# Kernel tuning notes

Hardware: AMD Instinct MI355X
Metric: run time of the kernel (lower is better)

The kernel has to match this reference:

```python
import jax, jax.numpy as jnp
import numpy as np

NUM_HEADS = 16


def _rope(x, c, s):
    # x: [T, H, D]; c, s: [T, D/2] -> rotate-half RoPE over full head_dim
    d2 = c.shape[-1]
    x1, x2 = x[..., :d2], x[..., d2:]
    c = c[:, None, :]
    s = s[:, None, :]
    return jnp.concatenate([x1 * c - x2 * s, x2 * c + x1 * s], axis=-1)


def setup_inputs() -> dict:
    key = jax.random.key(0)
    ks = jax.random.split(key, 4)
    B, L, dim = 8, 1024, 1024
    T = B * L
    D = dim // NUM_HEADS
    hidden_states = jax.random.normal(ks[0], (T, dim), dtype=jnp.float32)
    w_qkv = jax.random.normal(ks[1], (dim, 3 * dim), dtype=jnp.float32) * (dim ** -0.5)
    b_qkv = jnp.zeros((3 * dim,), dtype=jnp.float32)
    w_proj = jax.random.normal(ks[2], (dim, dim), dtype=jnp.float32) * (dim ** -0.5)
    b_proj = jnp.zeros((dim,), dtype=jnp.float32)
    # RoPE tables: positions restart at 0 for each packed sequence
    pos = jnp.tile(jnp.arange(L, dtype=jnp.float32), B)  # [T]
    inv_freq = 1.0 / (10000.0 ** (jnp.arange(0, D, 2, dtype=jnp.float32) / D))  # [D/2]
    freqs = pos[:, None] * inv_freq[None, :]  # [T, D/2]
    emb = jnp.concatenate([freqs, freqs], axis=-1)  # [T, D]
    cos = jnp.cos(emb)
    sin = jnp.sin(emb)
    cu_seqlens = (jnp.arange(B + 1, dtype=jnp.int32) * L)
    return {"hidden_states": hidden_states, "cos": cos, "sin": sin,
            "w_qkv": w_qkv, "b_qkv": b_qkv, "w_proj": w_proj, "b_proj": b_proj,
            "cu_seqlens": cu_seqlens}


def reference(hidden_states, cos, sin, w_qkv, b_qkv, w_proj, b_proj, cu_seqlens):
    T, dim = hidden_states.shape
    H = NUM_HEADS
    D = dim // H
    B = cu_seqlens.shape[0] - 1  # equal-length packed sequences
    L = T // B

    qkv = hidden_states @ w_qkv + b_qkv            # [T, 3*dim]
    qkv = qkv.reshape(T, 3, H, D)
    q, k, v = qkv[:, 0], qkv[:, 1], qkv[:, 2]       # [T, H, D]

    # module chunks cos/sin in half along last dim before apply_rotary_emb
    c = cos[..., : D // 2].astype(jnp.float32)
    s = sin[..., : D // 2].astype(jnp.float32)
    q = _rope(q.astype(jnp.float32), c, s).astype(hidden_states.dtype)
    k = _rope(k.astype(jnp.float32), c, s).astype(hidden_states.dtype)

    # varlen flash attention == block-diagonal attention; equal lengths -> reshape
    qb = q.reshape(B, L, H, D)
    kb = k.reshape(B, L, H, D)
    vb = v.reshape(B, L, H, D)
    scale = D ** -0.5
    scores = jnp.einsum("bqhd,bkhd->bhqk", qb, kb) * scale  # [B, H, L, L]
    probs = jax.nn.softmax(scores, axis=-1)
    out = jnp.einsum("bhqk,bkhd->bqhd", probs, vb)           # [B, L, H, D]
    out = out.reshape(T, dim)
    return out @ w_proj + b_proj
```

## Files before the change

### kernel.cpp

```cpp
#include <hip/hip_runtime.h>

typedef unsigned short ushort_t;
typedef __attribute__((ext_vector_type(8))) short short8;
typedef __attribute__((ext_vector_type(4))) float f32x4;

#define AS1 __attribute__((address_space(1)))
#define AS3 __attribute__((address_space(3)))

__device__ __forceinline__ ushort_t f2bf(float f) {
  unsigned int u = __builtin_bit_cast(unsigned int, f);
  u += 0x7fffu + ((u >> 16) & 1u);
  return (ushort_t)(u >> 16);
}

__device__ __forceinline__ unsigned int pack_bf2(float a, float b) {
  unsigned int ua = __builtin_bit_cast(unsigned int, a) + 0x8000u;
  unsigned int ub = __builtin_bit_cast(unsigned int, b) + 0x8000u;
  return (ua >> 16) | (ub & 0xffff0000u);
}

__device__ __forceinline__ void load_lds16(const ushort_t* g, ushort_t* l) {
  __builtin_amdgcn_global_load_lds((AS1 void*)g, (AS3 void*)l, 16, 0, 0);
}

#define MFMA16(a, b, c) __builtin_amdgcn_mfma_f32_16x16x32_bf16((a), (b), (c), 0, 0, 0)

__global__ __launch_bounds__(256) void k_convert(const float* __restrict__ src,
                                                 ushort_t* __restrict__ dst, int n8) {
  int i = blockIdx.x * 256 + threadIdx.x;
  if (i >= n8) return;
  const float4* s4 = (const float4*)src;
  float4 a = s4[(size_t)i * 2], b = s4[(size_t)i * 2 + 1];
  short8 o;
  o[0] = (short)f2bf(a.x); o[1] = (short)f2bf(a.y);
  o[2] = (short)f2bf(a.z); o[3] = (short)f2bf(a.w);
  o[4] = (short)f2bf(b.x); o[5] = (short)f2bf(b.y);
  o[6] = (short)f2bf(b.z); o[7] = (short)f2bf(b.w);
  *(short8*)(dst + (size_t)i * 8) = o;
}

__global__ __launch_bounds__(256) void k_transpose_w(const float* __restrict__ wqkv,
                                                     ushort_t* __restrict__ wqkvT,
                                                     const float* __restrict__ wproj,
                                                     ushort_t* __restrict__ wprojT) {
  __shared__ ushort_t t[64 * 65];
  const float* src;
  ushort_t* dst;
  int C, bx;
  if (blockIdx.x < 48) { src = wqkv; dst = wqkvT; C = 3072; bx = blockIdx.x; }
  else { src = wproj; dst = wprojT; C = 1024; bx = blockIdx.x - 48; }
  const int R = 1024;
  const int x0 = bx * 64, y0 = blockIdx.y * 64;
  const int c = threadIdx.x & 63, r0 = threadIdx.x >> 6;
#pragma unroll
  for (int i = 0; i < 16; ++i) {
    int r = r0 + i * 4;
    t[c * 65 + r] = f2bf(src[(size_t)(y0 + r) * C + x0 + c]);
  }
  __syncthreads();
#pragma unroll
  for (int i = 0; i < 16; ++i) {
    int rr = r0 + i * 4;
    dst[(size_t)(x0 + rr) * R + y0 + c] = t[rr * 65 + c];
  }
}

__global__ __launch_bounds__(512) void k_qkv_gemm_rope(
    const ushort_t* __restrict__ A, const ushort_t* __restrict__ Bt,
    const float* __restrict__ bias, const float* __restrict__ cosb,
    const float* __restrict__ sinb, ushort_t* __restrict__ Qb,
    ushort_t* __restrict__ Kb, ushort_t* __restrict__ Vp) {
  constexpr int K = 1024;
  __shared__ __align__(16) ushort_t As[256 * 64];
  __shared__ __align__(16) ushort_t Bs[128 * 64];
  const int tid = threadIdx.x, lane = tid & 63, wave = tid >> 6;
  const int quad = lane >> 4, ml = lane & 15;
  const int wm = wave & 3, wn = wave >> 2;
  const int m0 = blockIdx.y * 256, n0 = blockIdx.x * 128;
  f32x4 acc[4][4] = {};

  for (int kt = 0; kt < K / 64; ++kt) {
    __syncthreads();
    {
      const int kk0 = kt * 64;
#pragma unroll
      for (int i = 0; i < 4; ++i) {
        int cch = i * 512 + tid;
        int r = cch >> 3, s = cch & 7, gs = s ^ (r & 7);
        load_lds16(A + (size_t)(m0 + r) * K + kk0 + gs * 8, As + cch * 8);
      }
#pragma unroll
      for (int i = 0; i < 2; ++i) {
        int cch = i * 512 + tid;
        int r = cch >> 3, s = cch & 7, gs = s ^ (r & 7);
        load_lds16(Bt + (size_t)(n0 + r) * K + kk0 + gs * 8, Bs + cch * 8);
      }
    }
    __syncthreads();
#pragma unroll
    for (int ks = 0; ks < 2; ++ks) {
      short8 af[4], bfr[4];
#pragma unroll
      for (int mb = 0; mb < 4; ++mb) {
        int row = wm * 64 + mb * 16 + ml;
        int gs = (ks * 4 + quad) ^ (row & 7);
        af[mb] = *(const short8*)(As + row * 64 + gs * 8);
      }
#pragma unroll
      for (int nb = 0; nb < 4; ++nb) {
        int row = wn * 64 + nb * 16 + ml;
        int gs = (ks * 4 + quad) ^ (row & 7);
        bfr[nb] = *(const short8*)(Bs + row * 64 + gs * 8);
      }
#pragma unroll
      for (int mb = 0; mb < 4; ++mb)
#pragma unroll
        for (int nb = 0; nb < 4; ++nb)
          acc[mb][nb] = MFMA16(af[mb], bfr[nb], acc[mb][nb]);
    }
  }

  const int ncol0 = n0 + wn * 64;
  const int sec = ncol0 >> 10;
  const int h = (ncol0 & 1023) >> 6;
  if (sec < 2) {
    ushort_t* dst = (sec == 0) ? Qb : Kb;
#pragma unroll
    for (int mb = 0; mb < 4; ++mb) {
#pragma unroll
      for (int rg = 0; rg < 4; ++rg) {
        const int m = m0 + wm * 64 + mb * 16 + quad * 4 + rg;
        const int b = m >> 10, l = m & 1023;
        const size_t ob = ((size_t)(b * 16 + h) * 1024 + l) * 64;
#pragma unroll
        for (int nb = 0; nb < 2; ++nb) {
          const int d = nb * 16 + ml;
          float x1 = acc[mb][nb][rg] + bias[ncol0 + d];
          float x2 = acc[mb][nb + 2][rg] + bias[ncol0 + d + 32];
          float cv = cosb[(size_t)m * 64 + d];
          float sv = sinb[(size_t)m * 64 + d];
          dst[ob + d] = f2bf(x1 * cv - x2 * sv);
          dst[ob + d + 32] = f2bf(x2 * cv + x1 * sv);
        }
      }
    }
  } else {
    const int mrow = m0 + wm * 64;
    const int b = mrow >> 10, lB = mrow & 1023;
    ushort_t* vb = Vp + ((size_t)(b * 16 + h)) * 65536 + lB;
#pragma unroll
    for (int rg = 0; rg < 4; ++rg) {
#pragma unroll
      for (int nb = 0; nb < 4; ++nb) {
        const int d = nb * 16 + ml;
        const float bs = bias[ncol0 + d];
        uint2 w;
        w.x = pack_bf2(acc[0][nb][rg] + bs, acc[1][nb][rg] + bs);
        w.y = pack_bf2(acc[2][nb][rg] + bs, acc[3][nb][rg] + bs);
        *(uint2*)(vb + (size_t)d * 1024 + 16 * quad + 4 * rg) = w;
      }
    }
  }
}

__global__ __launch_bounds__(256, 4) void k_attn(const ushort_t* __restrict__ Qb,
                                                 const ushort_t* __restrict__ Kb,
                                                 const ushort_t* __restrict__ Vp,
                                                 ushort_t* __restrict__ Ob) {
  __shared__ __align__(16) ushort_t QP[9216];
  __shared__ __align__(16) ushort_t Ks[64 * 64];
  __shared__ __align__(16) ushort_t Vts[64 * 64];
  const int tid = threadIdx.x, lane = tid & 63, wave = tid >> 6;
  const int quad = lane >> 4, ml = lane & 15;
  const int bh = blockIdx.x & 127, qt = blockIdx.x >> 7;
  const int q0 = qt * 128;
  const size_t base = (size_t)bh * 65536;
  const float CEXP = 0.18033688011112042f;

#pragma unroll
  for (int i = 0; i < 4; ++i) {
    int cch = i * 256 + tid;
    int r = cch >> 3, s = cch & 7, gs = s ^ (r & 7);
    load_lds16(Qb + base + (size_t)(q0 + r) * 64 + gs * 8, QP + cch * 8);
  }
  __syncthreads();

  short8 qf[2][2];
#pragma unroll
  for (int mb = 0; mb < 2; ++mb)
#pragma unroll
    for (int ks = 0; ks < 2; ++ks) {
      int row = wave * 32 + mb * 16 + ml;
      int gs = (ks * 4 + quad) ^ (row & 7);
      qf[mb][ks] = *(const short8*)(QP + row * 64 + gs * 8);
    }

  ushort_t* Pw = QP + wave * 2304;
  f32x4 Oacc[2][4] = {};
  float lsum[2][4] = {};

  for (int kt = 0; kt < 16; ++kt) {
    __syncthreads();
#pragma unroll
    for (int i = 0; i < 2; ++i) {
      int cch = i * 256 + tid;
      int r = cch >> 3, s = cch & 7, gs = s ^ (r & 7);
      load_lds16(Kb + base + (size_t)(kt * 64 + r) * 64 + gs * 8, Ks + cch * 8);
    }
#pragma unroll
    for (int i = 0; i < 2; ++i) {
      int cch = i * 256 + tid;
      int r = cch >> 3, s = cch & 7, gs = s ^ (r & 7);
      load_lds16(Vp + base + (size_t)r * 1024 + kt * 64 + gs * 8, Vts + cch * 8);
    }
    __syncthreads();

    f32x4 Sacc[2][4] = {};
#pragma unroll
    for (int nb = 0; nb < 4; ++nb)
#pragma unroll
      for (int ks = 0; ks < 2; ++ks) {
        int row = nb * 16 + ml;
        int gs = (ks * 4 + quad) ^ (row & 7);
        short8 kf = *(const short8*)(Ks + row * 64 + gs * 8);
        Sacc[0][nb] = MFMA16(qf[0][ks], kf, Sacc[0][nb]);
        Sacc[1][nb] = MFMA16(qf[1][ks], kf, Sacc[1][nb]);
      }

#pragma unroll
    for (int mb = 0; mb < 2; ++mb) {
#pragma unroll
      for (int rg = 0; rg < 4; ++rg) {
        float p0 = exp2f(Sacc[mb][0][rg] * CEXP);
        float p1 = exp2f(Sacc[mb][1][rg] * CEXP);
        float p2 = exp2f(Sacc[mb][2][rg] * CEXP);
        float p3 = exp2f(Sacc[mb][3][rg] * CEXP);
        lsum[mb][rg] += (p0 + p1) + (p2 + p3);
        uint2 w;
        w.x = pack_bf2(p0, p1);
        w.y = pack_bf2(p2, p3);
        *(uint2*)(Pw + (mb * 16 + quad * 4 + rg) * 72 + ml * 4) = w;
      }
    }

#pragma unroll
    for (int ks = 0; ks < 2; ++ks) {
      short8 pf[2];
#pragma unroll
      for (int mb = 0; mb < 2; ++mb)
        pf[mb] = *(const short8*)(Pw + (mb * 16 + ml) * 72 + ks * 32 + quad * 8);
#pragma unroll
      for (int nb = 0; nb < 4; ++nb) {
        int row = nb * 16 + ml;
        int gs = (ks * 4 + quad) ^ (row & 7);
        short8 vf = *(const short8*)(Vts + row * 64 + gs * 8);
        Oacc[0][nb] = MFMA16(pf[0], vf, Oacc[0][nb]);
        Oacc[1][nb] = MFMA16(pf[1], vf, Oacc[1][nb]);
      }
    }
  }

  const int b = bh >> 4, h = bh & 15;
#pragma unroll
  for (int mb = 0; mb < 2; ++mb) {
#pragma unroll
    for (int rg = 0; rg < 4; ++rg) {
      float l = lsum[mb][rg];
      l += __shfl_xor(l, 1);
      l += __shfl_xor(l, 2);
      l += __shfl_xor(l, 4);
      l += __shfl_xor(l, 8);
      float inv = 1.f / l;
      int q = q0 + wave * 32 + mb * 16 + quad * 4 + rg;
      size_t ob = ((size_t)(b * 1024 + q)) * 1024 + h * 64;
#pragma unroll
      for (int nb = 0; nb < 4; ++nb)
        Ob[ob + nb * 16 + ml] = f2bf(Oacc[mb][nb][rg] * inv);
    }
  }
}

__global__ __launch_bounds__(256) void k_proj_gemm(const ushort_t* __restrict__ A,
                                                   const ushort_t* __restrict__ Bt,
                                                   const float* __restrict__ bias,
                                                   float* __restrict__ out) {
  constexpr int K = 1024;
  __shared__ __align__(16) ushort_t As[128 * 64];
  __shared__ __align__(16) ushort_t Bs[128 * 64];
  const int tid = threadIdx.x, lane = tid & 63, wave = tid >> 6;
  const int quad = lane >> 4, ml = lane & 15;
  const int wm = wave & 1, wn = wave >> 1;
  const int m0 = blockIdx.y * 128, n0 = blockIdx.x * 128;
  f32x4 acc[4][4] = {};

  for (int kt = 0; kt < K / 64; ++kt) {
    __syncthreads();
    {
      const int kk0 = kt * 64;
#pragma unroll
      for (int i = 0; i < 4; ++i) {
        int cch = i * 256 + tid;
        int r = cch >> 3, s = cch & 7, gs = s ^ (r & 7);
        load_lds16(A + (size_t)(m0 + r) * K + kk0 + gs * 8, As + cch * 8);
        load_lds16(Bt + (size_t)(n0 + r) * K + kk0 + gs * 8, Bs + cch * 8);
      }
    }
    __syncthreads();
#pragma unroll
    for (int ks = 0; ks < 2; ++ks) {
      short8 af[4], bfr[4];
#pragma unroll
      for (int mb = 0; mb < 4; ++mb) {
        int row = wm * 64 + mb * 16 + ml;
        int gs = (ks * 4 + quad) ^ (row & 7);
        af[mb] = *(const short8*)(As + row * 64 + gs * 8);
      }
#pragma unroll
      for (int nb = 0; nb < 4; ++nb) {
        int row = wn * 64 + nb * 16 + ml;
        int gs = (ks * 4 + quad) ^ (row & 7);
        bfr[nb] = *(const short8*)(Bs + row * 64 + gs * 8);
      }
#pragma unroll
      for (int mb = 0; mb < 4; ++mb)
#pragma unroll
        for (int nb = 0; nb < 4; ++nb)
          acc[mb][nb] = MFMA16(af[mb], bfr[nb], acc[mb][nb]);
    }
  }
#pragma unroll
  for (int mb = 0; mb < 4; ++mb) {
#pragma unroll
    for (int rg = 0; rg < 4; ++rg) {
      const int m = m0 + wm * 64 + mb * 16 + quad * 4 + rg;
#pragma unroll
      for (int nb = 0; nb < 4; ++nb) {
        const int n = n0 + wn * 64 + nb * 16 + ml;
        out[(size_t)m * 1024 + n] = acc[mb][nb][rg] + bias[n];
      }
    }
  }
}

extern "C" void kernel_launch(void* const* d_in, const int* in_sizes, int n_in,
                              void* d_out, int out_size, void* d_ws, size_t ws_size,
                              hipStream_t stream) {
  const float* hs = (const float*)d_in[0];
  const float* cosb = (const float*)d_in[1];
  const float* sinb = (const float*)d_in[2];
  const float* wqkv = (const float*)d_in[3];
  const float* bqkv = (const float*)d_in[4];
  const float* wproj = (const float*)d_in[5];
  const float* bproj = (const float*)d_in[6];
  float* out = (float*)d_out;

  char* ws = (char*)d_ws;
  ushort_t* hsb = (ushort_t*)(ws);
  ushort_t* wqkvT = (ushort_t*)(ws + (16u << 20));
  ushort_t* wprojT = (ushort_t*)(ws + (22u << 20));
  ushort_t* Qb = (ushort_t*)(ws + (24u << 20));
  ushort_t* Kb = (ushort_t*)(ws + (40u << 20));
  ushort_t* Vp = (ushort_t*)(ws + (56u << 20));
  ushort_t* attnb = hsb;

  k_convert<<<4096, 256, 0, stream>>>(hs, hsb, 1048576);
  k_transpose_w<<<dim3(64, 16), 256, 0, stream>>>(wqkv, wqkvT, wproj, wprojT);
  k_qkv_gemm_rope<<<dim3(24, 32), 512, 0, stream>>>(hsb, wqkvT, bqkv, cosb, sinb,
                                                    Qb, Kb, Vp);
  k_attn<<<1024, 256, 0, stream>>>(Qb, Kb, Vp, attnb);
  k_proj_gemm<<<dim3(8, 64), 256, 0, stream>>>(attnb, wprojT, bproj, out);
}
```

Measured before the change: 257.3 us.

## Fold softmax scale into Q RoPE, use hardware exp2/bf16 pack, hoist attention addressing

Multiplies the softmax exponent constant into the Q RoPE cos/sin in the QKV epilogue so the attention loop no longer multiplies each score. The exp2 call becomes the raw hardware exp2 builtin and the bf16 pair pack becomes the hardware cvt_pk instruction when available. Global and LDS addresses for the K/V loads and fragment reads are precomputed before the loop and advanced by pointer increments. The aim is fewer VALU instructions in the attention inner loop. The risks are scaling Q before bf16 rounding, which changes numerics slightly, and extra registers held by the hoisted pointers.

After: 245.1 us. 4.8% less time.

```diff
diff --git a/kernel.cpp b/kernel.cpp
--- a/kernel.cpp
+++ b/kernel.cpp
@@ -17,6 +17,33 @@
   unsigned int ua = __builtin_bit_cast(unsigned int, a) + 0x8000u;
   unsigned int ub = __builtin_bit_cast(unsigned int, b) + 0x8000u;
   return (ua >> 16) | (ub & 0xffff0000u);
+}
+
+#if defined(__has_builtin)
+#if __has_builtin(__builtin_amdgcn_cvt_pk_bf16_f32)
+#define HAVE_CVT_PK_BF16 1
+#endif
+#if __has_builtin(__builtin_amdgcn_exp2f)
+#define HAVE_EXP2 1
+#endif
+#endif
+
+__device__ __forceinline__ unsigned int pack2(float a, float b) {
+#ifdef HAVE_CVT_PK_BF16
+  typedef __attribute__((ext_vector_type(2))) __bf16 bf2_t;
+  bf2_t r = __builtin_amdgcn_cvt_pk_bf16_f32(a, b);
+  return __builtin_bit_cast(unsigned int, r);
+#else
+  return pack_bf2(a, b);
+#endif
+}
+
+__device__ __forceinline__ float fast_exp2(float x) {
+#ifdef HAVE_EXP2
+  return __builtin_amdgcn_exp2f(x);
+#else
+  return exp2f(x);
+#endif
 }
 
 __device__ __forceinline__ void load_lds16(const ushort_t* g, ushort_t* l) {
@@ -125,6 +152,7 @@
   const int h = (ncol0 & 1023) >> 6;
   if (sec < 2) {
     ushort_t* dst = (sec == 0) ? Qb : Kb;
+    const float qs = (sec == 0) ? 0.18033688011112042f : 1.0f;
 #pragma unroll
     for (int mb = 0; mb < 4; ++mb) {
 #pragma unroll
@@ -137,8 +165,8 @@
           const int d = nb * 16 + ml;
           float x1 = acc[mb][nb][rg] + bias[ncol0 + d];
           float x2 = acc[mb][nb + 2][rg] + bias[ncol0 + d + 32];
-          float cv = cosb[(size_t)m * 64 + d];
-          float sv = sinb[(size_t)m * 64 + d];
+          float cv = cosb[(size_t)m * 64 + d] * qs;
+          float sv = sinb[(size_t)m * 64 + d] * qs;
           dst[ob + d] = f2bf(x1 * cv - x2 * sv);
           dst[ob + d + 32] = f2bf(x2 * cv + x1 * sv);
         }
@@ -175,7 +203,6 @@
   const int bh = blockIdx.x & 127, qt = blockIdx.x >> 7;
   const int q0 = qt * 128;
   const size_t base = (size_t)bh * 65536;
-  const float CEXP = 0.18033688011112042f;
 
 #pragma unroll
   for (int i = 0; i < 4; ++i) {
@@ -196,6 +223,38 @@
     }
 
   ushort_t* Pw = QP + wave * 2304;
+
+  const ushort_t* kg[2];
+  const ushort_t* vg[2];
+  ushort_t *kl[2], *vl[2];
+#pragma unroll
+  for (int i = 0; i < 2; ++i) {
+    int cch = i * 256 + tid;
+    int r = cch >> 3, gs = (cch & 7) ^ (r & 7);
+    kg[i] = Kb + base + (size_t)r * 64 + gs * 8;
+    kl[i] = Ks + cch * 8;
+    vg[i] = Vp + base + (size_t)r * 1024 + gs * 8;
+    vl[i] = Vts + cch * 8;
+  }
+  const ushort_t* kfp[4][2];
+  const ushort_t* vfp[4][2];
+#pragma unroll
+  for (int nb = 0; nb < 4; ++nb)
+#pragma unroll
+    for (int ks = 0; ks < 2; ++ks) {
+      int row = nb * 16 + ml;
+      int gs = (ks * 4 + quad) ^ (row & 7);
+      kfp[nb][ks] = Ks + row * 64 + gs * 8;
+      vfp[nb][ks] = Vts + row * 64 + gs * 8;
+    }
+  const ushort_t* pfp[2][2];
+#pragma unroll
+  for (int mb = 0; mb < 2; ++mb)
+#pragma unroll
+    for (int ks = 0; ks < 2; ++ks)
+      pfp[mb][ks] = Pw + (mb * 16 + ml) * 72 + ks * 32 + quad * 8;
+  ushort_t* pwb = Pw + quad * 288 + ml * 4;
+
   f32x4 Oacc[2][4] = {};
   float lsum[2][4] = {};
 
@@ -203,15 +262,8 @@
     __syncthreads();
 #pragma unroll
     for (int i = 0; i < 2; ++i) {
-      int cch = i * 256 + tid;
-      int r = cch >> 3, s = cch & 7, gs = s ^ (r & 7);
-      load_lds16(Kb + base + (size_t)(kt * 64 + r) * 64 + gs * 8, Ks + cch * 8);
-    }
-#pragma unroll
-    for (int i = 0; i < 2; ++i) {
-      int cch = i * 256 + tid;
-      int r = cch >> 3, s = cch & 7, gs = s ^ (r & 7);
-      load_lds16(Vp + base + (size_t)r * 1024 + kt * 64 + gs * 8, Vts + cch * 8);
+      load_lds16(kg[i], kl[i]); kg[i] += 4096;
+      load_lds16(vg[i], vl[i]); vg[i] += 64;
     }
     __syncthreads();
 
@@ -220,9 +272,7 @@
     for (int nb = 0; nb < 4; ++nb)
 #pragma unroll
       for (int ks = 0; ks < 2; ++ks) {
-        int row = nb * 16 + ml;
-        int gs = (ks * 4 + quad) ^ (row & 7);
-        short8 kf = *(const short8*)(Ks + row * 64 + gs * 8);
+        short8 kf = *(const short8*)kfp[nb][ks];
         Sacc[0][nb] = MFMA16(qf[0][ks], kf, Sacc[0][nb]);
         Sacc[1][nb] = MFMA16(qf[1][ks], kf, Sacc[1][nb]);
       }
@@ -231,31 +281,27 @@
     for (int mb = 0; mb < 2; ++mb) {
 #pragma unroll
       for (int rg = 0; rg < 4; ++rg) {
-        float p0 = exp2f(Sacc[mb][0][rg] * CEXP);
-        float p1 = exp2f(Sacc[mb][1][rg] * CEXP);
-        float p2 = exp2f(Sacc[mb][2][rg] * CEXP);
-        float p3 = exp2f(Sacc[mb][3][rg] * CEXP);
+        float p0 = fast_exp2(Sacc[mb][0][rg]);
+        float p1 = fast_exp2(Sacc[mb][1][rg]);
+        float p2 = fast_exp2(Sacc[mb][2][rg]);
+        float p3 = fast_exp2(Sacc[mb][3][rg]);
         lsum[mb][rg] += (p0 + p1) + (p2 + p3);
         uint2 w;
-        w.x = pack_bf2(p0, p1);
-        w.y = pack_bf2(p2, p3);
-        *(uint2*)(Pw + (mb * 16 + quad * 4 + rg) * 72 + ml * 4) = w;
+        w.x = pack2(p0, p1);
+        w.y = pack2(p2, p3);
+        *(uint2*)(pwb + mb * 1152 + rg * 72) = w;
       }
     }
 
 #pragma unroll
     for (int ks = 0; ks < 2; ++ks) {
-      short8 pf[2];
-#pragma unroll
-      for (int mb = 0; mb < 2; ++mb)
-        pf[mb] = *(const short8*)(Pw + (mb * 16 + ml) * 72 + ks * 32 + quad * 8);
+      short8 pf0 = *(const short8*)pfp[0][ks];
+      short8 pf1 = *(const short8*)pfp[1][ks];
 #pragma unroll
       for (int nb = 0; nb < 4; ++nb) {
-        int row = nb * 16 + ml;
-        int gs = (ks * 4 + quad) ^ (row & 7);
-        short8 vf = *(const short8*)(Vts + row * 64 + gs * 8);
-        Oacc[0][nb] = MFMA16(pf[0], vf, Oacc[0][nb]);
-        Oacc[1][nb] = MFMA16(pf[1], vf, Oacc[1][nb]);
+        short8 vf = *(const short8*)vfp[nb][ks];
+        Oacc[0][nb] = MFMA16(pf0, vf, Oacc[0][nb]);
+        Oacc[1][nb] = MFMA16(pf1, vf, Oacc[1][nb]);
       }
     }
   }
```
